# Kernel tuning notes

Hardware: AMD Instinct MI355X
Metric: run time of the kernel (lower is better)

The kernel has to match this reference:

```python
import jax, jax.numpy as jnp
import numpy as np

LAM = 1e-05
NUM_POINTS = 300
THRESHOLD = 0.5


def _sobel(img):
    # img: [B, 1, H, W] -> edge magnitude [B, 1, H, W]
    kx = jnp.array([[-1., 0., 1.], [-2., 0., 2.], [-1., 0., 1.]], jnp.float32).reshape(1, 1, 3, 3)
    ky = jnp.array([[-1., -2., -1.], [0., 0., 0.], [1., 2., 1.]], jnp.float32).reshape(1, 1, 3, 3)
    dn = jax.lax.conv_dimension_numbers(img.shape, kx.shape, ('NCHW', 'OIHW', 'NCHW'))
    ex = jax.lax.conv_general_dilated(img, kx, (1, 1), ((1, 1), (1, 1)), dimension_numbers=dn)
    ey = jax.lax.conv_general_dilated(img, ky, (1, 1), ((1, 1), (1, 1)), dimension_numbers=dn)
    return jnp.sqrt(ex ** 2 + ey ** 2)


def _select_points(edge_map, key):
    # JIT-friendly analogue of nonzero + randperm[:300]: random scores on
    # above-threshold pixels, take top NUM_POINTS; invalid slots are padded
    # with a duplicate of the first valid point (zero-length MST edges, so
    # they contribute nothing to total persistence, matching fewer points).
    H, W = edge_map.shape
    flat = edge_map.reshape(-1)
    mask = flat > THRESHOLD
    scores = jnp.where(mask, jax.random.uniform(key, flat.shape), -jnp.inf)
    _, idx = jax.lax.top_k(scores, NUM_POINTS)
    valid = mask[idx]
    pts = jnp.stack([idx // W, idx % W], axis=-1).astype(jnp.float32)  # (row, col)
    pts = jnp.where(valid[:, None], pts, pts[0])
    return pts


def _mst_total_persistence(pts):
    # H0 persistence of a Vietoris-Rips complex: births are 0, deaths are the
    # MST edge lengths (Prim's algorithm via lax.scan over N-1 steps).
    # total_persistence with exponent q=2: sum(death^2).
    d2 = jnp.sum((pts[:, None, :] - pts[None, :, :]) ** 2, axis=-1)
    D = jnp.sqrt(jnp.maximum(d2, 0.0))  # [N, N]
    n = pts.shape[0]
    in_tree = jnp.zeros((n,), dtype=bool).at[0].set(True)

    def step(carry, _):
        in_tree, mind = carry
        m = jnp.where(in_tree, jnp.inf, mind)
        j = jnp.argmin(m)
        w = m[j]
        in_tree = in_tree.at[j].set(True)
        mind = jnp.minimum(mind, D[j])
        return (in_tree, mind), w

    _, deaths = jax.lax.scan(step, (in_tree, D[0]), None, length=n - 1)
    return jnp.sum(deaths ** 2)


def _topo_loss(model_output, labels):
    pred_edges = _sobel(jax.nn.sigmoid(model_output))[:, 0]  # [B, H, W]
    mask_edges = _sobel(labels)[:, 0]                         # [B, H, W]
    B = pred_edges.shape[0]
    keys = jax.random.split(jax.random.key(42), 2 * B).reshape(B, 2)

    def per_sample(pe, me, k):
        pts_p = _select_points(pe, k[0])
        pts_m = _select_points(me, k[1])
        tp_p = _mst_total_persistence(pts_p)
        tp_m = _mst_total_persistence(pts_m)
        # SummaryStatisticLoss(total_persistence): |stat(mask) - stat(pred)|
        return jnp.abs(tp_m - tp_p)

    losses = jax.vmap(per_sample)(pred_edges, mask_edges, keys)
    return LAM * jnp.sum(losses) / B


def setup_inputs() -> dict:
    key = jax.random.key(0)
    k1, k2 = jax.random.split(key)
    model_output = jax.random.normal(k1, (32, 1, 512, 512), dtype=jnp.float32)
    labels = jax.random.uniform(k2, (32, 1, 512, 512), dtype=jnp.float32)
    return {"model_output": model_output, "labels": labels}


def reference(model_output, labels):
    return _topo_loss(model_output, labels)
```

## Files before the change

kernel.cpp:

```cpp
#include <hip/hip_runtime.h>
#include <cstdint>
#include <cstddef>

#define NPIX (512 * 512)
#define NMAPS 64
#define NPTS 300
#define CAP 2048
#define SLOTS 32
#define LBUFSZ 64
#define NWORDS 4096
#define TARGET 700.0
#define MT_BITS 0xFF63C000u

__device__ __forceinline__ uint32_t umin32(uint32_t a, uint32_t b) {
  return a < b ? a : b;
}

__device__ __forceinline__ uint32_t rotl32(uint32_t x, int r) {
  return (x << r) | (x >> (32 - r));
}

__device__ __forceinline__ void tf2x32(uint32_t k0, uint32_t k1,
                                       uint32_t x0, uint32_t x1,
                                       uint32_t& o0, uint32_t& o1) {
  uint32_t ks2 = k0 ^ k1 ^ 0x1BD11BDAu;
#define TFR(r) { x0 += x1; x1 = rotl32(x1, r); x1 ^= x0; }
  x0 += k0; x1 += k1;
  TFR(13) TFR(15) TFR(26) TFR(6)
  x0 += k1; x1 += ks2 + 1u;
  TFR(17) TFR(29) TFR(16) TFR(24)
  x0 += ks2; x1 += k0 + 2u;
  TFR(13) TFR(15) TFR(26) TFR(6)
  x0 += k0; x1 += k1 + 3u;
  TFR(17) TFR(29) TFR(16) TFR(24)
  x0 += k1; x1 += ks2 + 4u;
  TFR(13) TFR(15) TFR(26) TFR(6)
  x0 += ks2; x1 += k0 + 5u;
#undef TFR
  o0 = x0; o1 = x1;
}

__device__ __forceinline__ void tf4(uint32_t k0, uint32_t k1, uint32_t pb,
                                    uint32_t& z0, uint32_t& z1, uint32_t& z2,
                                    uint32_t& z3) {
  const uint32_t ks2 = k0 ^ k1 ^ 0x1BD11BDAu;
  const uint32_t s = pb + k1;
  uint32_t a0 = k0, a1 = s;
  uint32_t b0 = k0, b1 = s + 1u;
  uint32_t c0 = k0, c1 = s + 2u;
  uint32_t d0 = k0, d1 = s + 3u;
#define R4(r)                                                         \
  a0 += a1; b0 += b1; c0 += c1; d0 += d1;                             \
  a1 = rotl32(a1, r); b1 = rotl32(b1, r);                             \
  c1 = rotl32(c1, r); d1 = rotl32(d1, r);                             \
  a1 ^= a0; b1 ^= b0; c1 ^= c0; d1 ^= d0;
#define K4(ka, kb)                                                    \
  a0 += (ka); b0 += (ka); c0 += (ka); d0 += (ka);                     \
  a1 += (kb); b1 += (kb); c1 += (kb); d1 += (kb);
  R4(13) R4(15) R4(26) R4(6)  K4(k1, ks2 + 1u)
  R4(17) R4(29) R4(16) R4(24) K4(ks2, k0 + 2u)
  R4(13) R4(15) R4(26) R4(6)  K4(k0, k1 + 3u)
  R4(17) R4(29) R4(16) R4(24) K4(k1, ks2 + 4u)
  R4(13) R4(15) R4(26) R4(6)  K4(ks2, k0 + 5u)
#undef R4
#undef K4
  z0 = a0 ^ a1; z1 = b0 ^ b1; z2 = c0 ^ c1; z3 = d0 ^ d1;
}

__device__ __forceinline__ uint32_t score23(uint32_t k0, uint32_t k1, uint32_t p) {
  uint32_t a, b;
  tf2x32(k0, k1, 0u, p, a, b);
  return (a ^ b) >> 9;
}

__device__ __forceinline__ void map_key(int m, uint32_t& k0, uint32_t& k1) {
  tf2x32(0u, 42u, 0u, (uint32_t)m, k0, k1);
}

template <int CTRL>
__device__ __forceinline__ uint32_t dpp_mov_u32(uint32_t x) {
  return (uint32_t)__builtin_amdgcn_update_dpp((int)x, (int)x, CTRL, 0xF, 0xF,
                                               false);
}

template <int CTRL>
__device__ __forceinline__ uint32_t dpp_or0(uint32_t x) {
  return (uint32_t)__builtin_amdgcn_update_dpp(0, (int)x, CTRL, 0xF, 0xF,
                                               false);
}

template <int CTRL>
__device__ __forceinline__ float dpp_mov_f32(float x) {
  return __uint_as_float(dpp_mov_u32<CTRL>(__float_as_uint(x)));
}

__device__ __forceinline__ uint32_t wave_min_u32_bcast(uint32_t v) {
  v = umin32(v, dpp_mov_u32<0x111>(v));
  v = umin32(v, dpp_mov_u32<0x112>(v));
  v = umin32(v, dpp_mov_u32<0x114>(v));
  v = umin32(v, dpp_mov_u32<0x118>(v));
  v = umin32(v, dpp_mov_u32<0x142>(v));
  v = umin32(v, dpp_mov_u32<0x143>(v));
  return (uint32_t)__builtin_amdgcn_readlane((int)v, 63);
}

template <bool PRED, bool YIN>
__device__ __forceinline__ float4 ld4row(const float* __restrict__ src,
                                         int row, int X0) {
  if constexpr (!YIN) {
    if ((unsigned)row >= 512u) return make_float4(0.f, 0.f, 0.f, 0.f);
  }
  float4 v = *reinterpret_cast<const float4*>(src + (size_t)row * 512 + X0);
  if constexpr (PRED) {
    v.x = 1.f / (1.f + __expf(-v.x));
    v.y = 1.f / (1.f + __expf(-v.y));
    v.z = 1.f / (1.f + __expf(-v.z));
    v.w = 1.f / (1.f + __expf(-v.w));
  }
  return v;
}

template <bool PRED, bool YIN>
__device__ __forceinline__ float ldhrow(const float* __restrict__ src,
                                        int row, int hx, bool hact) {
  if (!hact) return 0.f;
  if constexpr (!YIN) {
    if ((unsigned)row >= 512u) return 0.f;
  }
  float t = src[(size_t)row * 512 + hx];
  if constexpr (PRED) t = 1.f / (1.f + __expf(-t));
  return t;
}

__device__ __forceinline__ void push_surv(unsigned long long* lbuf,
                                          unsigned int* lcnt, uint32_t x,
                                          uint32_t p) {
  unsigned int pos = atomicAdd(lcnt, 1u);
  if (pos < LBUFSZ)
    lbuf[pos] = ((unsigned long long)(x >> 9) << 32) | (uint32_t)(~p);
}

template <bool PRED, bool YIN>
__device__ __forceinline__ void part_body(
    const float* __restrict__ src, unsigned long long* __restrict__ bitmap,
    unsigned int* __restrict__ wcnts, unsigned long long* lbuf,
    unsigned int* lcnt, int m, int l, int h, int qq, uint32_t k0,
    uint32_t k1) {
  const int y0 = qq * 4;
  const int X0 = h * 256 + l * 4;
  const int lr = l & 15;
  const int hx = (lr == 0) ? (X0 - 1) : (X0 + 4);
  const bool hact = ((lr == 0) || (lr == 15)) && ((unsigned)hx < 512u);

  float4 fA = ld4row<PRED, YIN>(src, y0 - 1, X0);
  float4 fB = ld4row<PRED, YIN>(src, y0 + 0, X0);
  float4 fC = ld4row<PRED, YIN>(src, y0 + 1, X0);
  float4 fD = ld4row<PRED, YIN>(src, y0 + 2, X0);
  float sA = ldhrow<PRED, YIN>(src, y0 - 1, hx, hact);
  float sB = ldhrow<PRED, YIN>(src, y0 + 0, hx, hact);
  float sC = ldhrow<PRED, YIN>(src, y0 + 1, hx, hact);
  float sD = ldhrow<PRED, YIN>(src, y0 + 2, hx, hact);

  unsigned int cnt = 0;
  unsigned long long* __restrict__ bm2 =
      bitmap + (size_t)m * NWORDS + (size_t)y0 * 8 + (h * 4 + (l >> 4));
  uint32_t pbase = (uint32_t)(y0 * 512 + X0);

#define ROWQ(RA, RB, RC, SA, SB, SC, II)                                      \
  do {                                                                        \
    float t0 = RA.x + 2.f * RB.x + RC.x, t1 = RA.y + 2.f * RB.y + RC.y;       \
    float t2 = RA.z + 2.f * RB.z + RC.z, t3 = RA.w + 2.f * RB.w + RC.w;       \
    float u0 = RC.x - RA.x, u1 = RC.y - RA.y;                                 \
    float u2 = RC.z - RA.z, u3 = RC.w - RA.w;                                 \
    float th = SA + 2.f * SB + SC, uh = SC - SA;                              \
    float tU = dpp_mov_f32<0x111>(t3);          \
    float uU = dpp_mov_f32<0x111>(u3);                                        \
    float tD = dpp_mov_f32<0x101>(t0);          \
    float uD = dpp_mov_f32<0x101>(u0);                                        \
    if (lr == 0) { tU = th; uU = uh; }                                        \
    if (lr == 15) { tD = th; uD = uh; }                                       \
    float ex0 = t1 - tU, ex1 = t2 - t0, ex2 = t3 - t1, ex3 = tD - t2;         \
    float ey0 = uU + 2.f * u0 + u1, ey1 = u0 + 2.f * u1 + u2;                 \
    float ey2 = u1 + 2.f * u2 + u3, ey3 = u2 + 2.f * u3 + uD;                 \
    uint32_t nib = (ex0 * ex0 + ey0 * ey0 > 0.25f ? 1u : 0u) |                \
                   (ex1 * ex1 + ey1 * ey1 > 0.25f ? 2u : 0u) |                \
                   (ex2 * ex2 + ey2 * ey2 > 0.25f ? 4u : 0u) |                \
                   (ex3 * ex3 + ey3 * ey3 > 0.25f ? 8u : 0u);                 \
    uint32_t z0, z1, z2, z3;                                                  \
    tf4(k0, k1, pbase, z0, z1, z2, z3);                                       \
    uint32_t qm = (z0 >= MT_BITS ? 1u : 0u) | (z1 >= MT_BITS ? 2u : 0u) |     \
                  (z2 >= MT_BITS ? 4u : 0u) | (z3 >= MT_BITS ? 8u : 0u);      \
    uint32_t sv = nib & qm;                                                   \
    if (sv) {                                                                 \
      if (sv & 1u) push_surv(lbuf, lcnt, z0, pbase);                          \
      if (sv & 2u) push_surv(lbuf, lcnt, z1, pbase + 1u);                     \
      if (sv & 4u) push_surv(lbuf, lcnt, z2, pbase + 2u);                     \
      if (sv & 8u) push_surv(lbuf, lcnt, z3, pbase + 3u);                     \
    }                                                                         \
    unsigned long long full = (unsigned long long)nib << (4 * lr);            \
    uint32_t wlo = (uint32_t)full, whi = (uint32_t)(full >> 32);              \
    wlo |= dpp_or0<0x111>(wlo); whi |= dpp_or0<0x111>(whi);                   \
    wlo |= dpp_or0<0x112>(wlo); whi |= dpp_or0<0x112>(whi);                   \
    wlo |= dpp_or0<0x114>(wlo); whi |= dpp_or0<0x114>(whi);                   \
    wlo |= dpp_or0<0x118>(wlo); whi |= dpp_or0<0x118>(whi);                   \
    if (lr == 15) {                                                           \
      unsigned long long word = ((unsigned long long)whi << 32) | wlo;        \
      bm2[(II) * 8] = word;                                                   \
      cnt += (unsigned int)__popcll(word);                                    \
    }                                                                         \
    pbase += 512u;                                                            \
  } while (0)

  ROWQ(fA, fB, fC, sA, sB, sC, 0);
  fA = ld4row<PRED, YIN>(src, y0 + 3, X0);
  sA = ldhrow<PRED, YIN>(src, y0 + 3, hx, hact);
  ROWQ(fB, fC, fD, sB, sC, sD, 1);
  fB = ld4row<PRED, YIN>(src, y0 + 4, X0);
  sB = ldhrow<PRED, YIN>(src, y0 + 4, hx, hact);
  ROWQ(fC, fD, fA, sC, sD, sA, 2);
  ROWQ(fD, fA, fB, sD, sA, sB, 3);
#undef ROWQ

  cnt += __shfl_xor(cnt, 16);
  cnt += __shfl_xor(cnt, 32);
  if (l == 15) wcnts[m * 256 + 2 * qq + h] = cnt;
}

__global__ __launch_bounds__(256) void edge_collect_kernel(
    const float* __restrict__ mo, const float* __restrict__ lb,
    unsigned long long* __restrict__ bitmap, unsigned int* __restrict__ wcnts,
    unsigned long long* __restrict__ cand, unsigned int* __restrict__ bcnt,
    float* __restrict__ out) {
  const int b = blockIdx.x;
  const int s = b >> 6;
  const int j = b & 63;
  const int v = threadIdx.x >> 6;
  const int l = threadIdx.x & 63;
  const int h = v & 1;
  const int qq = 2 * j + (v >> 1);
  const int mA = 2 * s;
  const int mB = 2 * s + 1;
  const float* __restrict__ srcP = mo + (size_t)s * NPIX;
  const float* __restrict__ srcM = lb + (size_t)s * NPIX;

  if (b == 0 && threadIdx.x == 0) out[0] = 0.f;

  __shared__ unsigned long long lbufP[LBUFSZ], lbufM[LBUFSZ];
  __shared__ unsigned int lcntP, lcntM;
  if (threadIdx.x == 0) { lcntP = 0; lcntM = 0; }
  __syncthreads();

  uint32_t ka0, ka1, kb0, kb1;
  map_key(mA, ka0, ka1);
  map_key(mB, kb0, kb1);
  ka0 = (uint32_t)__builtin_amdgcn_readfirstlane((int)ka0);
  ka1 = (uint32_t)__builtin_amdgcn_readfirstlane((int)ka1);
  kb0 = (uint32_t)__builtin_amdgcn_readfirstlane((int)kb0);
  kb1 = (uint32_t)__builtin_amdgcn_readfirstlane((int)kb1);

  const bool yin = (qq != 0) && (qq != 127);
  if (yin) {
    part_body<true, true>(srcP, bitmap, wcnts, lbufP, &lcntP, mA, l, h, qq, ka0, ka1);
    part_body<false, true>(srcM, bitmap, wcnts, lbufM, &lcntM, mB, l, h, qq, kb0, kb1);
  } else {
    part_body<true, false>(srcP, bitmap, wcnts, lbufP, &lcntP, mA, l, h, qq, ka0, ka1);
    part_body<false, false>(srcM, bitmap, wcnts, lbufM, &lcntM, mB, l, h, qq, kb0, kb1);
  }

  __syncthreads();
  const unsigned int tP = lcntP, tM = lcntM;
  const unsigned int ccP = tP < SLOTS ? tP : SLOTS;
  const unsigned int ccM = tM < SLOTS ? tM : SLOTS;
  for (unsigned int i = threadIdx.x; i < ccP; i += 256)
    cand[(size_t)mA * CAP + j * SLOTS + i] = lbufP[i];
  for (unsigned int i = threadIdx.x; i < ccM; i += 256)
    cand[(size_t)mB * CAP + j * SLOTS + i] = lbufM[i];
  if (threadIdx.x == 0) {
    bcnt[mA * 64 + j] = tP;
    bcnt[mB * 64 + j] = tM;
  }
}

__device__ __forceinline__ void reduce_N(const unsigned int* __restrict__ wcnts,
                                         int m, int tid, unsigned int* sN) {
  if (tid < 64) {
    const unsigned int* w = wcnts + m * 256;
    unsigned int v = w[tid] + w[tid + 64] + w[tid + 128] + w[tid + 192];
#pragma unroll
    for (int off = 32; off > 0; off >>= 1) v += __shfl_xor(v, off, 64);
    if (tid == 0) *sN = v;
  }
}

__global__ __launch_bounds__(256) void select_kernel(
    const unsigned long long* __restrict__ bitmap,
    const unsigned int* __restrict__ wcnts,
    const unsigned long long* __restrict__ cand,
    const unsigned int* __restrict__ bcnt,
    uint32_t* __restrict__ pts, unsigned int* __restrict__ nsel) {
  const int m = blockIdx.x;
  const int tid = threadIdx.x;
  __shared__ unsigned long long buf[CAP];
  __shared__ unsigned int hist[256];
  __shared__ unsigned int scnt64[64];
  __shared__ unsigned int sbase[65];
  __shared__ unsigned int s_tot, s_cnt, s_b, s_rank, sN, s_ovf;

  reduce_N(wcnts, m, tid, &sN);
  if (tid < 64) scnt64[tid] = bcnt[m * 64 + tid];
  __syncthreads();
  const unsigned int N = sN;
  if (N == 0) { if (tid == 0) nsel[m] = 0; return; }
  const unsigned int need = N < NPTS ? N : NPTS;

  if (tid == 0) {
    unsigned int s = 0, ovf = 0;
    for (int i = 0; i < 64; ++i) {
      sbase[i] = s;
      unsigned int cg = scnt64[i];
      if (cg > SLOTS) ovf = 1;
      s += cg < SLOTS ? cg : SLOTS;
    }
    sbase[64] = s;
    s_ovf = ovf;
  }
  __syncthreads();

  unsigned int c;
  if (!s_ovf && sbase[64] >= need) {
    c = sbase[64];
    const int g = tid >> 2, j0 = tid & 3;
    const unsigned int cg = scnt64[g] < SLOTS ? scnt64[g] : SLOTS;
    for (unsigned int i = j0; i < cg; i += 4)
      buf[sbase[g] + i] = cand[(size_t)m * CAP + g * SLOTS + i];
    __syncthreads();
  } else {
    uint32_t k0, k1;
    map_key(m, k0, k1);
    const unsigned long long* __restrict__ wmap = bitmap + (size_t)m * NWORDS;
    unsigned int mt = 0, cnt = 0;
    double target = TARGET;
    for (int iter = 0; iter < 16; ++iter) {
      mt = ((double)N > target)
               ? (unsigned int)(8388608.0 * (1.0 - target / (double)N))
               : 0u;
      if (tid == 0) s_tot = 0;
      __syncthreads();
      unsigned int lc = 0;
      for (int w = tid; w < NWORDS; w += 256) {
        unsigned long long word = wmap[w];
        while (word) {
          int bpos = __builtin_ctzll(word);
          word &= word - 1;
          uint32_t p = ((uint32_t)w << 6) + (uint32_t)bpos;
          lc += (score23(k0, k1, p) >= mt) ? 1u : 0u;
        }
      }
      if (lc) atomicAdd(&s_tot, lc);
      __syncthreads();
      cnt = s_tot;
      __syncthreads();
      if (cnt >= need && cnt <= CAP) break;
      if (cnt < need) target *= 3.0; else target *= 0.5;
    }
    if (tid == 0) s_cnt = 0;
    __syncthreads();
    for (int w = tid; w < NWORDS; w += 256) {
      unsigned long long word = wmap[w];
      while (word) {
        int bpos = __builtin_ctzll(word);
        word &= word - 1;
        uint32_t p = ((uint32_t)w << 6) + (uint32_t)bpos;
        uint32_t sc = score23(k0, k1, p);
        if (sc >= mt) {
          unsigned int pos = atomicAdd(&s_cnt, 1u);
          if (pos < CAP)
            buf[pos] = ((unsigned long long)sc << 32) | (uint32_t)(~p);
        }
      }
    }
    __syncthreads();
    c = s_cnt < CAP ? s_cnt : CAP;
    __syncthreads();
  }

  unsigned long long T = 0ull;
  if (c > need) {
    unsigned int rank = need;
    unsigned long long prefix = 0ull;
    for (int sh = 48; sh >= 0; sh -= 8) {
      hist[tid] = 0;
      __syncthreads();
      for (unsigned int i = tid; i < c; i += 256) {
        unsigned long long k = buf[i];
        if ((k >> (sh + 8)) == (prefix >> (sh + 8)))
          atomicAdd(&hist[(unsigned int)(k >> sh) & 255u], 1u);
      }
      __syncthreads();
      if (tid < 64) {
        unsigned int h0 = hist[4 * tid], h1 = hist[4 * tid + 1];
        unsigned int h2 = hist[4 * tid + 2], h3 = hist[4 * tid + 3];
        unsigned int gsum = h0 + h1 + h2 + h3;
        unsigned int s = gsum;
#pragma unroll
        for (int off = 1; off < 64; off <<= 1) {
          unsigned int o = __shfl_down(s, off, 64);
          s += (tid + off < 64) ? o : 0u;
        }
        unsigned int above = s - gsum;
        unsigned int S3 = above, S2 = S3 + h3, S1 = S2 + h2, S0 = S1 + h1;
        if (S3 < rank && rank <= S3 + h3) { s_b = 4 * tid + 3; s_rank = rank - S3; }
        if (S2 < rank && rank <= S2 + h2) { s_b = 4 * tid + 2; s_rank = rank - S2; }
        if (S1 < rank && rank <= S1 + h1) { s_b = 4 * tid + 1; s_rank = rank - S1; }
        if (S0 < rank && rank <= S0 + h0) { s_b = 4 * tid + 0; s_rank = rank - S0; }
      }
      __syncthreads();
      prefix |= ((unsigned long long)s_b) << sh;
      rank = s_rank;
    }
    T = prefix;
  }

  if (tid == 0) s_cnt = 0;
  __syncthreads();
  for (unsigned int i = tid; i < c; i += 256) {
    unsigned long long k = buf[i];
    if (k >= T) {
      unsigned int pos = atomicAdd(&s_cnt, 1u);
      if (pos < NPTS) {
        uint32_t p = ~(uint32_t)k;
        pts[(size_t)m * NPTS + pos] = ((p >> 9) << 16) | (p & 511u);
      }
    }
  }
  __syncthreads();
  if (tid == 0) nsel[m] = s_cnt < need ? s_cnt : need;
}

__global__ __launch_bounds__(128, 1) void mst_kernel(
    const uint32_t* __restrict__ pts, const unsigned int* __restrict__ nsel,
    float* __restrict__ out) {
  const int wv = threadIdx.x >> 6;
  const int m = blockIdx.x * 2 + wv;
  const int l = threadIdx.x & 63;
  const int n = (int)nsel[m];
  __shared__ float stp[2];

  unsigned int utp = 0;
  if (n > 1) {
    uint32_t pk[5], key[5];
    int px[5], py[5];
#pragma unroll
    for (int k = 0; k < 5; ++k) {
      int id = k * 64 + l;
      pk[k] = (id < n) ? pts[(size_t)m * NPTS + id] : 0u;
    }
    const uint32_t p0 = (uint32_t)__builtin_amdgcn_readlane((int)pk[0], 0);
    const int x0 = (int)(p0 >> 16), y0 = (int)(p0 & 0xFFFFu);
#pragma unroll
    for (int k = 0; k < 5; ++k) {
      int id = k * 64 + l;
      px[k] = (int)(pk[k] >> 16);
      py[k] = (int)(pk[k] & 0xFFFFu);
      if (id > 0 && id < n) {
        int dx = px[k] - x0, dy = py[k] - y0;
        key[k] = ((uint32_t)(__mul24(dx, dx) + __mul24(dy, dy)) << 9) |
                 (uint32_t)id;
      } else {
        key[k] = 0xFFFFFFFFu;
      }
    }

    for (int it = 0; it < n - 1; ++it) {
      uint32_t best = umin32(umin32(umin32(key[0], key[1]),
                                    umin32(key[2], key[3])), key[4]);
      best = wave_min_u32_bcast(best);
      utp += best >> 9;
      const int j = (int)(best & 511u);
      const int ko = j >> 6, lo = j & 63;
      uint32_t cp = pk[0];
#pragma unroll
      for (int k = 1; k < 5; ++k) cp = (ko == k) ? pk[k] : cp;
      const uint32_t pj = (uint32_t)__builtin_amdgcn_readlane((int)cp, lo);
      const int jx = (int)(pj >> 16), jy = (int)(pj & 0xFFFFu);
#pragma unroll
      for (int k = 0; k < 5; ++k) {
        int dx = px[k] - jx, dy = py[k] - jy;
        uint32_t nk = ((uint32_t)(__mul24(dx, dx) + __mul24(dy, dy)) << 9) |
                      (uint32_t)(k * 64 + l);
        uint32_t upd =
            (key[k] == 0xFFFFFFFFu) ? 0xFFFFFFFFu : umin32(key[k], nk);
        key[k] = (k == ko && l == lo) ? 0xFFFFFFFFu : upd;
      }
    }
  }
  if (l == 0) stp[wv] = (float)utp;
  __syncthreads();
  if (threadIdx.x == 0)
    atomicAdd(out, 1e-5f * fabsf(stp[1] - stp[0]) / 32.f);
}

extern "C" void kernel_launch(void* const* d_in, const int* in_sizes, int n_in,
                              void* d_out, int out_size, void* d_ws,
                              size_t ws_size, hipStream_t stream) {
  const float* mo = (const float*)d_in[0];
  const float* lb = (const float*)d_in[1];
  float* out = (float*)d_out;
  char* ws = (char*)d_ws;

  unsigned long long* bitmap = (unsigned long long*)ws;
  unsigned long long* cand = (unsigned long long*)(ws + 2097152);
  unsigned int* wcnts = (unsigned int*)(ws + 3145728);
  unsigned int* bcnt  = (unsigned int*)(ws + 3211264);
  unsigned int* nsel  = (unsigned int*)(ws + 3227648);
  uint32_t* pts       = (uint32_t*)(ws + 3227904);

  edge_collect_kernel<<<2048, 256, 0, stream>>>(mo, lb, bitmap, wcnts,
                                                cand, bcnt, out);
  select_kernel<<<NMAPS, 256, 0, stream>>>(bitmap, wcnts, cand, bcnt, pts,
                                           nsel);
  mst_kernel<<<32, 128, 0, stream>>>(pts, nsel, out);
}
```

Before: 216.0 us.

## Fuse point selection and MST into one kernel using shared memory

Merges the select and MST kernels into a single kernel where each block selects points for both maps of a sample in turn, keeps them in shared memory, then runs Prim's MST on two waves. This removes one kernel launch and the global round trip for selected points and counts. In exchange the selection now runs over 32 blocks instead of 64, with the two maps handled one after another, which halves parallelism for that stage. An extra barrier is added in the radix-select loop.

```diff
diff --git a/kernel.cpp b/kernel.cpp
--- a/kernel.cpp
+++ b/kernel.cpp
@@ -281,8 +281,16 @@
   }
 }
 
-__device__ __forceinline__ void reduce_N(const unsigned int* __restrict__ wcnts,
-                                         int m, int tid, unsigned int* sN) {
+__device__ void select_body(
+    int m, int tid,
+    const unsigned long long* __restrict__ bitmap,
+    const unsigned int* __restrict__ wcnts,
+    const unsigned long long* __restrict__ cand,
+    const unsigned int* __restrict__ bcnt,
+    unsigned long long* buf, unsigned int* hist, unsigned int* scnt64,
+    unsigned int* sbase, unsigned int* s_tot, unsigned int* s_cnt,
+    unsigned int* s_b, unsigned int* s_rank, unsigned int* sN,
+    unsigned int* s_ovf, uint32_t* pts_sh, unsigned int* nsel_out) {
   if (tid < 64) {
     const unsigned int* w = wcnts + m * 256;
     unsigned int v = w[tid] + w[tid + 64] + w[tid + 128] + w[tid + 192];
@@ -290,27 +298,10 @@
     for (int off = 32; off > 0; off >>= 1) v += __shfl_xor(v, off, 64);
     if (tid == 0) *sN = v;
   }
-}
-
-__global__ __launch_bounds__(256) void select_kernel(
-    const unsigned long long* __restrict__ bitmap,
-    const unsigned int* __restrict__ wcnts,
-    const unsigned long long* __restrict__ cand,
-    const unsigned int* __restrict__ bcnt,
-    uint32_t* __restrict__ pts, unsigned int* __restrict__ nsel) {
-  const int m = blockIdx.x;
-  const int tid = threadIdx.x;
-  __shared__ unsigned long long buf[CAP];
-  __shared__ unsigned int hist[256];
-  __shared__ unsigned int scnt64[64];
-  __shared__ unsigned int sbase[65];
-  __shared__ unsigned int s_tot, s_cnt, s_b, s_rank, sN, s_ovf;
-
-  reduce_N(wcnts, m, tid, &sN);
   if (tid < 64) scnt64[tid] = bcnt[m * 64 + tid];
   __syncthreads();
-  const unsigned int N = sN;
-  if (N == 0) { if (tid == 0) nsel[m] = 0; return; }
+  const unsigned int N = *sN;
+  if (N == 0) { if (tid == 0) *nsel_out = 0; return; }
   const unsigned int need = N < NPTS ? N : NPTS;
 
   if (tid == 0) {
@@ -322,12 +313,12 @@
       s += cg < SLOTS ? cg : SLOTS;
     }
     sbase[64] = s;
-    s_ovf = ovf;
+    *s_ovf = ovf;
   }
   __syncthreads();
 
   unsigned int c;
-  if (!s_ovf && sbase[64] >= need) {
+  if (!(*s_ovf) && sbase[64] >= need) {
     c = sbase[64];
     const int g = tid >> 2, j0 = tid & 3;
     const unsigned int cg = scnt64[g] < SLOTS ? scnt64[g] : SLOTS;
@@ -344,7 +335,7 @@
       mt = ((double)N > target)
                ? (unsigned int)(8388608.0 * (1.0 - target / (double)N))
                : 0u;
-      if (tid == 0) s_tot = 0;
+      if (tid == 0) *s_tot = 0;
       __syncthreads();
       unsigned int lc = 0;
       for (int w = tid; w < NWORDS; w += 256) {
@@ -356,14 +347,14 @@
           lc += (score23(k0, k1, p) >= mt) ? 1u : 0u;
         }
       }
-      if (lc) atomicAdd(&s_tot, lc);
-      __syncthreads();
-      cnt = s_tot;
+      if (lc) atomicAdd(s_tot, lc);
+      __syncthreads();
+      cnt = *s_tot;
       __syncthreads();
       if (cnt >= need && cnt <= CAP) break;
       if (cnt < need) target *= 3.0; else target *= 0.5;
     }
-    if (tid == 0) s_cnt = 0;
+    if (tid == 0) *s_cnt = 0;
     __syncthreads();
     for (int w = tid; w < NWORDS; w += 256) {
       unsigned long long word = wmap[w];
@@ -373,14 +364,14 @@
         uint32_t p = ((uint32_t)w << 6) + (uint32_t)bpos;
         uint32_t sc = score23(k0, k1, p);
         if (sc >= mt) {
-          unsigned int pos = atomicAdd(&s_cnt, 1u);
+          unsigned int pos = atomicAdd(s_cnt, 1u);
           if (pos < CAP)
             buf[pos] = ((unsigned long long)sc << 32) | (uint32_t)(~p);
         }
       }
     }
     __syncthreads();
-    c = s_cnt < CAP ? s_cnt : CAP;
+    c = *s_cnt < CAP ? *s_cnt : CAP;
     __syncthreads();
   }
 
@@ -409,94 +400,117 @@
         }
         unsigned int above = s - gsum;
         unsigned int S3 = above, S2 = S3 + h3, S1 = S2 + h2, S0 = S1 + h1;
-        if (S3 < rank && rank <= S3 + h3) { s_b = 4 * tid + 3; s_rank = rank - S3; }
-        if (S2 < rank && rank <= S2 + h2) { s_b = 4 * tid + 2; s_rank = rank - S2; }
-        if (S1 < rank && rank <= S1 + h1) { s_b = 4 * tid + 1; s_rank = rank - S1; }
-        if (S0 < rank && rank <= S0 + h0) { s_b = 4 * tid + 0; s_rank = rank - S0; }
-      }
-      __syncthreads();
-      prefix |= ((unsigned long long)s_b) << sh;
-      rank = s_rank;
+        if (S3 < rank && rank <= S3 + h3) { *s_b = 4 * tid + 3; *s_rank = rank - S3; }
+        if (S2 < rank && rank <= S2 + h2) { *s_b = 4 * tid + 2; *s_rank = rank - S2; }
+        if (S1 < rank && rank <= S1 + h1) { *s_b = 4 * tid + 1; *s_rank = rank - S1; }
+        if (S0 < rank && rank <= S0 + h0) { *s_b = 4 * tid + 0; *s_rank = rank - S0; }
+      }
+      __syncthreads();
+      prefix |= ((unsigned long long)(*s_b)) << sh;
+      rank = *s_rank;
+      __syncthreads();
     }
     T = prefix;
   }
 
-  if (tid == 0) s_cnt = 0;
+  if (tid == 0) *s_cnt = 0;
   __syncthreads();
   for (unsigned int i = tid; i < c; i += 256) {
     unsigned long long k = buf[i];
     if (k >= T) {
-      unsigned int pos = atomicAdd(&s_cnt, 1u);
+      unsigned int pos = atomicAdd(s_cnt, 1u);
       if (pos < NPTS) {
         uint32_t p = ~(uint32_t)k;
-        pts[(size_t)m * NPTS + pos] = ((p >> 9) << 16) | (p & 511u);
+        pts_sh[pos] = ((p >> 9) << 16) | (p & 511u);
       }
     }
   }
   __syncthreads();
-  if (tid == 0) nsel[m] = s_cnt < need ? s_cnt : need;
-}
-
-__global__ __launch_bounds__(128, 1) void mst_kernel(
-    const uint32_t* __restrict__ pts, const unsigned int* __restrict__ nsel,
-    float* __restrict__ out) {
-  const int wv = threadIdx.x >> 6;
-  const int m = blockIdx.x * 2 + wv;
-  const int l = threadIdx.x & 63;
-  const int n = (int)nsel[m];
+  if (tid == 0) *nsel_out = *s_cnt < need ? *s_cnt : need;
+}
+
+__global__ __launch_bounds__(256) void select_mst_kernel(
+    const unsigned long long* __restrict__ bitmap,
+    const unsigned int* __restrict__ wcnts,
+    const unsigned long long* __restrict__ cand,
+    const unsigned int* __restrict__ bcnt, float* __restrict__ out) {
+  __shared__ unsigned long long buf[CAP];
+  __shared__ unsigned int hist[256];
+  __shared__ unsigned int scnt64[64];
+  __shared__ unsigned int sbase[65];
+  __shared__ unsigned int s_tot, s_cnt, s_b, s_rank, sN, s_ovf;
+  __shared__ uint32_t pts_sh[2][NPTS];
+  __shared__ unsigned int nsel_sh[2];
   __shared__ float stp[2];
 
-  unsigned int utp = 0;
-  if (n > 1) {
-    uint32_t pk[5], key[5];
-    int px[5], py[5];
-#pragma unroll
-    for (int k = 0; k < 5; ++k) {
-      int id = k * 64 + l;
-      pk[k] = (id < n) ? pts[(size_t)m * NPTS + id] : 0u;
-    }
-    const uint32_t p0 = (uint32_t)__builtin_amdgcn_readlane((int)pk[0], 0);
-    const int x0 = (int)(p0 >> 16), y0 = (int)(p0 & 0xFFFFu);
-#pragma unroll
-    for (int k = 0; k < 5; ++k) {
-      int id = k * 64 + l;
-      px[k] = (int)(pk[k] >> 16);
-      py[k] = (int)(pk[k] & 0xFFFFu);
-      if (id > 0 && id < n) {
-        int dx = px[k] - x0, dy = py[k] - y0;
-        key[k] = ((uint32_t)(__mul24(dx, dx) + __mul24(dy, dy)) << 9) |
-                 (uint32_t)id;
-      } else {
-        key[k] = 0xFFFFFFFFu;
-      }
-    }
-
-    for (int it = 0; it < n - 1; ++it) {
-      uint32_t best = umin32(umin32(umin32(key[0], key[1]),
-                                    umin32(key[2], key[3])), key[4]);
-      best = wave_min_u32_bcast(best);
-      utp += best >> 9;
-      const int j = (int)(best & 511u);
-      const int ko = j >> 6, lo = j & 63;
-      uint32_t cp = pk[0];
-#pragma unroll
-      for (int k = 1; k < 5; ++k) cp = (ko == k) ? pk[k] : cp;
-      const uint32_t pj = (uint32_t)__builtin_amdgcn_readlane((int)cp, lo);
-      const int jx = (int)(pj >> 16), jy = (int)(pj & 0xFFFFu);
+  const int b = blockIdx.x;
+  const int tid = threadIdx.x;
+
+  select_body(2 * b + 0, tid, bitmap, wcnts, cand, bcnt, buf, hist, scnt64,
+              sbase, &s_tot, &s_cnt, &s_b, &s_rank, &sN, &s_ovf,
+              pts_sh[0], &nsel_sh[0]);
+  __syncthreads();
+  select_body(2 * b + 1, tid, bitmap, wcnts, cand, bcnt, buf, hist, scnt64,
+              sbase, &s_tot, &s_cnt, &s_b, &s_rank, &sN, &s_ovf,
+              pts_sh[1], &nsel_sh[1]);
+  __syncthreads();
+
+  const int wv = tid >> 6;
+  const int l = tid & 63;
+  if (wv < 2) {
+    const int n = (int)nsel_sh[wv];
+    unsigned int utp = 0;
+    if (n > 1) {
+      uint32_t pk[5], key[5];
+      int px[5], py[5];
 #pragma unroll
       for (int k = 0; k < 5; ++k) {
-        int dx = px[k] - jx, dy = py[k] - jy;
-        uint32_t nk = ((uint32_t)(__mul24(dx, dx) + __mul24(dy, dy)) << 9) |
-                      (uint32_t)(k * 64 + l);
-        uint32_t upd =
-            (key[k] == 0xFFFFFFFFu) ? 0xFFFFFFFFu : umin32(key[k], nk);
-        key[k] = (k == ko && l == lo) ? 0xFFFFFFFFu : upd;
+        int id = k * 64 + l;
+        pk[k] = (id < n) ? pts_sh[wv][id] : 0u;
+      }
+      const uint32_t p0 = (uint32_t)__builtin_amdgcn_readlane((int)pk[0], 0);
+      const int x0 = (int)(p0 >> 16), y0 = (int)(p0 & 0xFFFFu);
+#pragma unroll
+      for (int k = 0; k < 5; ++k) {
+        int id = k * 64 + l;
+        px[k] = (int)(pk[k] >> 16);
+        py[k] = (int)(pk[k] & 0xFFFFu);
+        if (id > 0 && id < n) {
+          int dx = px[k] - x0, dy = py[k] - y0;
+          key[k] = ((uint32_t)(__mul24(dx, dx) + __mul24(dy, dy)) << 9) |
+                   (uint32_t)id;
+        } else {
+          key[k] = 0xFFFFFFFFu;
+        }
+      }
+
+      for (int it = 0; it < n - 1; ++it) {
+        uint32_t best = umin32(umin32(umin32(key[0], key[1]),
+                                      umin32(key[2], key[3])), key[4]);
+        best = wave_min_u32_bcast(best);
+        utp += best >> 9;
+        const int j = (int)(best & 511u);
+        const int ko = j >> 6, lo = j & 63;
+        uint32_t cp = pk[0];
+#pragma unroll
+        for (int k = 1; k < 5; ++k) cp = (ko == k) ? pk[k] : cp;
+        const uint32_t pj = (uint32_t)__builtin_amdgcn_readlane((int)cp, lo);
+        const int jx = (int)(pj >> 16), jy = (int)(pj & 0xFFFFu);
+#pragma unroll
+        for (int k = 0; k < 5; ++k) {
+          int dx = px[k] - jx, dy = py[k] - jy;
+          uint32_t nk = ((uint32_t)(__mul24(dx, dx) + __mul24(dy, dy)) << 9) |
+                        (uint32_t)(k * 64 + l);
+          uint32_t upd =
+              (key[k] == 0xFFFFFFFFu) ? 0xFFFFFFFFu : umin32(key[k], nk);
+          key[k] = (k == ko && l == lo) ? 0xFFFFFFFFu : upd;
+        }
       }
     }
-  }
-  if (l == 0) stp[wv] = (float)utp;
-  __syncthreads();
-  if (threadIdx.x == 0)
+    if (l == 0) stp[wv] = (float)utp;
+  }
+  __syncthreads();
+  if (tid == 0)
     atomicAdd(out, 1e-5f * fabsf(stp[1] - stp[0]) / 32.f);
 }
 
@@ -512,12 +526,8 @@
   unsigned long long* cand = (unsigned long long*)(ws + 2097152);
   unsigned int* wcnts = (unsigned int*)(ws + 3145728);
   unsigned int* bcnt  = (unsigned int*)(ws + 3211264);
-  unsigned int* nsel  = (unsigned int*)(ws + 3227648);
-  uint32_t* pts       = (uint32_t*)(ws + 3227904);
 
   edge_collect_kernel<<<2048, 256, 0, stream>>>(mo, lb, bitmap, wcnts,
                                                 cand, bcnt, out);
-  select_kernel<<<NMAPS, 256, 0, stream>>>(bitmap, wcnts, cand, bcnt, pts,
-                                           nsel);
-  mst_kernel<<<32, 128, 0, stream>>>(pts, nsel, out);
-}
+  select_mst_kernel<<<32, 256, 0, stream>>>(bitmap, wcnts, cand, bcnt, out);
+}
```

Measured after the change: 221.9 us. 2.7% more time.
